# Kernel optimization log

Hardware: AMD Instinct MI355X
Metric: run time of the kernel (lower is better)

The kernel has to match this reference:

```python
import jax, jax.numpy as jnp
import numpy as np

N = 50000   # nodes
E = 800000  # edges before self-loops
H = 4       # heads
D = 64      # num_h_feats (per-head out dim of hidden layers)
C = 2       # num_classes
NEG = 0.2   # DGL GATConv leaky_relu negative_slope
EPS = 1e-5  # BatchNorm eps


def setup_inputs() -> dict:
    key = jax.random.key(0)
    ks = jax.random.split(key, 16)
    inp = {}
    inp['feats'] = jax.random.normal(ks[0], (N, 9), jnp.float32)
    inp['W1'] = jax.random.normal(ks[1], (9, H * D), jnp.float32) * 0.1
    inp['al1'] = jax.random.normal(ks[2], (H, D), jnp.float32) * 0.1
    inp['ar1'] = jax.random.normal(ks[3], (H, D), jnp.float32) * 0.1
    inp['b1'] = jnp.zeros((H, D), jnp.float32)
    inp['Wm'] = jax.random.normal(ks[4], (D, H * D), jnp.float32) * 0.1
    inp['alm'] = jax.random.normal(ks[5], (H, D), jnp.float32) * 0.1
    inp['arm'] = jax.random.normal(ks[6], (H, D), jnp.float32) * 0.1
    inp['bm'] = jnp.zeros((H, D), jnp.float32)
    inp['W2'] = jax.random.normal(ks[7], (D, H * C), jnp.float32) * 0.1
    inp['al2'] = jax.random.normal(ks[8], (H, C), jnp.float32) * 0.1
    inp['ar2'] = jax.random.normal(ks[9], (H, C), jnp.float32) * 0.1
    inp['b2'] = jnp.zeros((H, C), jnp.float32)
    inp['gamma'] = jnp.ones((D,), jnp.float32)
    inp['beta'] = jnp.zeros((D,), jnp.float32)
    inp['src'] = jax.random.randint(ks[10], (E,), 0, N, jnp.int32)
    inp['dst'] = jax.random.randint(ks[11], (E,), 0, N, jnp.int32)
    return inp


def gat_layer(x, W, al, ar, b, src, dst, out_d):
    """DGL GATConv: linear -> per-edge attention -> dst-softmax -> scatter-sum."""
    n = x.shape[0]
    z = (x @ W).reshape(n, H, out_d)                 # [N, H, Dout]
    el = jnp.sum(z * al, axis=-1)                    # [N, H] attn on src
    er = jnp.sum(z * ar, axis=-1)                    # [N, H] attn on dst
    e = jax.nn.leaky_relu(el[src] + er[dst], NEG)    # [E, H]
    m = jax.ops.segment_max(e, dst, num_segments=n)  # per-dst max (stable softmax)
    a = jnp.exp(e - m[dst])
    s = jax.ops.segment_sum(a, dst, num_segments=n)
    alpha = a / s[dst]                               # [E, H]
    out = jax.ops.segment_sum(alpha[:, :, None] * z[src], dst, num_segments=n)
    return out + b                                   # [N, H, Dout]


def batchnorm(h, gamma, beta):
    mu = jnp.mean(h, axis=0)
    var = jnp.var(h, axis=0)
    return (h - mu) * jax.lax.rsqrt(var + EPS) * gamma + beta


def reference(feats, W1, al1, ar1, b1, Wm, alm, arm, bm, W2, al2, ar2, b2,
              gamma, beta, src, dst):
    # dgl.add_self_loop
    loop = jnp.arange(N, dtype=src.dtype)
    s = jnp.concatenate([src, loop])
    d = jnp.concatenate([dst, loop])
    h = gat_layer(feats, W1, al1, ar1, b1, s, d, D).sum(axis=1)  # head-sum
    h = batchnorm(h, gamma, beta)
    h = gat_layer(h, Wm, alm, arm, bm, s, d, D).sum(axis=1)
    h = batchnorm(h, gamma, beta)
    o = gat_layer(h, W2, al2, ar2, b2, s, d, C).sum(axis=1)      # [N, C]
    return o
```

## Files before the change

kernel.cpp:

```cpp
#include <hip/hip_runtime.h>
#include <hip/hip_bf16.h>

typedef __hip_bfloat16 bf16;
typedef __bf16 bf16x8 __attribute__((ext_vector_type(8)));
typedef float f32x4 __attribute__((ext_vector_type(4)));
typedef _Float16 h16;
typedef _Float16 h16x4 __attribute__((ext_vector_type(4)));

#define LOG2E 1.44269504088896340736f

__device__ __forceinline__ float b2f(bf16 v) { return __bfloat162float(v); }

__device__ __forceinline__ float ldin(const void* p, size_t i, int isb) {
    return isb ? b2f(((const bf16*)p)[i]) : ((const float*)p)[i];
}
__device__ __forceinline__ unsigned short f2bfbits(float f) {
    bf16 v = __float2bfloat16(f);
    return *(unsigned short*)&v;
}

__global__ __launch_bounds__(256) void prep_kernel(
    const void* __restrict__ feats, const void* __restrict__ W1, const void* __restrict__ Wm,
    const void* __restrict__ al1, const void* __restrict__ ar1,
    const void* __restrict__ alm, const void* __restrict__ arm,
    const unsigned* __restrict__ gbits,
    const int* __restrict__ dstv, int* __restrict__ deg,
    unsigned short* __restrict__ fpad, unsigned short* __restrict__ W1T,
    unsigned short* __restrict__ WmT,
    float* __restrict__ alf1, float* __restrict__ arf1,
    float* __restrict__ alfm, float* __restrict__ arfm,
    unsigned short* __restrict__ zhs, float* __restrict__ zcs, float* __restrict__ elp,
    int* __restrict__ flag, int Nn, int E) {
    int isb = (gbits[0] == 0x3F803F80u) ? 1 : 0;
    long t = (long)blockIdx.x * 256 + threadIdx.x;
    if (t == 0) *flag = isb;
    long b0 = (long)Nn * 8;
    long b1 = b0 + 2048;
    long b2 = b1 + 2048;
    long b3 = b2 + 256;
    long b4 = b3 + 268;
    long b5 = b4 + E;
    if (t < b0) {
        int s = (int)(t & 7); long n = t >> 3;
        int k0 = s * 8;
        union { unsigned short us[8]; uint4 v; } o;
#pragma unroll
        for (int j = 0; j < 8; j++) {
            int k = k0 + j;
            o.us[j] = (k < 9) ? f2bfbits(ldin(feats, (size_t)n * 9 + k, isb))
                              : (unsigned short)0;
        }
        *(uint4*)(fpad + t * 8) = o.v;
    } else if (t < b1) {
        long u = t - b0;
        int col = (int)(u >> 3), k0 = ((int)u & 7) * 8;
        union { unsigned short us[8]; uint4 v; } o;
#pragma unroll
        for (int j = 0; j < 8; j++) {
            int k = k0 + j;
            o.us[j] = (k < 9) ? f2bfbits(ldin(W1, (size_t)k * 256 + col, isb))
                              : (unsigned short)0;
        }
        *(uint4*)(W1T + u * 8) = o.v;
    } else if (t < b2) {
        long u = t - b1;
        int col = (int)(u >> 3), k0 = ((int)u & 7) * 8;
        union { unsigned short us[8]; uint4 v; } o;
#pragma unroll
        for (int j = 0; j < 8; j++) {
            int k = k0 + j;
            o.us[j] = f2bfbits(ldin(Wm, (size_t)k * 256 + col, isb));
        }
        *(uint4*)(WmT + u * 8) = o.v;
    } else if (t < b3) {
        int u = (int)(t - b2);
        alf1[u] = ldin(al1, u, isb) * LOG2E; arf1[u] = ldin(ar1, u, isb) * LOG2E;
        alfm[u] = ldin(alm, u, isb) * LOG2E; arfm[u] = ldin(arm, u, isb) * LOG2E;
    } else if (t < b4) {
        long u = t - b3;
        if (u < 4) {
            elp[(size_t)Nn * 4 + u] = -1e30f;
        } else if (u < 260) {
            zhs[(size_t)Nn * 256 + (u - 4)] = 0;
        } else {
            zcs[(size_t)Nn * 8 + (u - 260)] = 0.f;
        }
    } else if (t < b5) {
        atomicAdd(&deg[dstv[t - b4]], 1);
    }
}

__global__ __launch_bounds__(256) void scan1_kernel(
    const int* __restrict__ deg, int* __restrict__ off, int* __restrict__ bsum, int Nn) {
    __shared__ int s[256];
    int t = threadIdx.x, i = blockIdx.x * 256 + t;
    int v = (i < Nn) ? ((deg[i] + 3) & ~3) : 0;
    s[t] = v; __syncthreads();
#pragma unroll
    for (int o = 1; o < 256; o <<= 1) {
        int a = (t >= o) ? s[t - o] : 0;
        __syncthreads();
        s[t] += a;
        __syncthreads();
    }
    if (i < Nn) off[i] = s[t];
    if (t == 255) bsum[blockIdx.x] = s[255];
}

__global__ __launch_bounds__(256) void scan2_kernel(int* __restrict__ bsum, int NB) {
    __shared__ int s[256];
    int t = threadIdx.x;
    int v = (t < NB) ? bsum[t] : 0;
    s[t] = v; __syncthreads();
#pragma unroll
    for (int o = 1; o < 256; o <<= 1) {
        int a = (t >= o) ? s[t - o] : 0;
        __syncthreads();
        s[t] += a;
        __syncthreads();
    }
    if (t < NB) bsum[t] = s[t] - v;
}

__global__ __launch_bounds__(256) void scan3_kernel(
    const int* __restrict__ deg, int* __restrict__ off, int* __restrict__ cur,
    int* __restrict__ adj, const int* __restrict__ bsum, int Nn) {
    int i = blockIdx.x * 256 + threadIdx.x;
    if (i < Nn) {
        int d = deg[i], pd = (d + 3) & ~3;
        int ex = off[i] - pd + bsum[i >> 8];
        off[i] = ex;
        cur[i] = ex;
        for (int j = d; j < pd; j++) adj[ex + j] = Nn;
        if (i == Nn - 1) {
            int tot = ex + pd;
            off[Nn] = tot;
#pragma unroll
            for (int j = 0; j < 8; j++) adj[tot + j] = Nn;
        }
    }
}

__global__ __launch_bounds__(256) void scatter_kernel(
    const int* __restrict__ src, const int* __restrict__ dst,
    int* __restrict__ cur, int* __restrict__ adj, int E) {
    int t = blockIdx.x * 256 + threadIdx.x;
    if (t < E) {
        int p = atomicAdd(&cur[dst[t]], 1);
        adj[p] = src[t];
    }
}

__global__ __launch_bounds__(256) void lin_mfma_l1_kernel(
    const unsigned short* __restrict__ xb, const unsigned short* __restrict__ WT,
    const float* __restrict__ alf, const float* __restrict__ arf,
    h16* __restrict__ zh, float* __restrict__ el, float* __restrict__ er, int Nn) {
    __shared__ h16 zs[16 * 256];
    int w = threadIdx.x >> 6;
    int l = threadIdx.x & 63;
    int quad = l >> 4, lc = l & 15;
    int node0 = blockIdx.x * 16;

    int mrow = node0 + lc; if (mrow >= Nn) mrow = Nn - 1;
    const bf16x8* xa = (const bf16x8*)(xb + (size_t)mrow * 64);
    bf16x8 a0 = xa[quad];
    bf16x8 a1 = xa[quad + 4];

    float pe[4] = {0.f, 0.f, 0.f, 0.f}, pr[4] = {0.f, 0.f, 0.f, 0.f};
    int row0 = quad * 4;
#pragma unroll
    for (int ct = 0; ct < 4; ++ct) {
        int col = w * 64 + ct * 16 + lc;
        const bf16x8* wb = (const bf16x8*)(WT + (size_t)col * 64);
        bf16x8 b0 = wb[quad];
        bf16x8 b1 = wb[quad + 4];
        f32x4 c = {0.f, 0.f, 0.f, 0.f};
        c = __builtin_amdgcn_mfma_f32_16x16x32_bf16(a0, b0, c, 0, 0, 0);
        c = __builtin_amdgcn_mfma_f32_16x16x32_bf16(a1, b1, c, 0, 0, 0);
        float av = alf[col], rv = arf[col];
#pragma unroll
        for (int r = 0; r < 4; ++r) {
            pe[r] = fmaf(c[r], av, pe[r]);
            pr[r] = fmaf(c[r], rv, pr[r]);
            zs[(row0 + r) * 256 + col] = (h16)c[r];
        }
    }
#pragma unroll
    for (int o = 1; o < 16; o <<= 1) {
#pragma unroll
        for (int r = 0; r < 4; ++r) {
            pe[r] += __shfl_xor(pe[r], o);
            pr[r] += __shfl_xor(pr[r], o);
        }
    }
    if (lc == 0) {
#pragma unroll
        for (int r = 0; r < 4; ++r) {
            int n = node0 + row0 + r;
            if (n < Nn) { el[n * 4 + w] = pe[r]; er[n * 4 + w] = pr[r]; }
        }
    }
    __syncthreads();
#pragma unroll
    for (int it = 0; it < 2; ++it) {
        int flat = it * 2048 + threadIdx.x * 8;
        int row = flat >> 8;
        if (node0 + row < Nn)
            *(uint4*)(zh + (size_t)node0 * 256 + flat) = *(const uint4*)(zs + flat);
    }
}

__global__ __launch_bounds__(256) void lin_mfma_bn_kernel(
    const float* __restrict__ x,
    const float* __restrict__ bnsum, const float* __restrict__ bnsumsq,
    const void* __restrict__ gamma, const void* __restrict__ beta,
    const unsigned short* __restrict__ WT,
    const float* __restrict__ alf, const float* __restrict__ arf,
    h16* __restrict__ zh, float* __restrict__ el, float* __restrict__ er,
    const int* __restrict__ flag, int Nn) {
    __shared__ h16 zs[16 * 256];
    __shared__ __align__(16) float scs[64], shs[64];
    int tid = threadIdx.x;
    if (tid < 64) {
        int isb = *flag;
        float inv_n = 1.f / (float)Nn;
        float mu = bnsum[tid] * inv_n;
        float var = bnsumsq[tid] * inv_n - mu * mu;
        float s = rsqrtf(var + 1e-5f) * ldin(gamma, tid, isb);
        scs[tid] = s;
        shs[tid] = ldin(beta, tid, isb) - mu * s;
    }
    __syncthreads();

    int w = tid >> 6;
    int l = tid & 63;
    int quad = l >> 4, lc = l & 15;
    int node0 = blockIdx.x * 16;

    int mrow = node0 + lc; if (mrow >= Nn) mrow = Nn - 1;
    const float* xr = x + (size_t)mrow * 64 + quad * 8;
    float4 f0 = ((const float4*)xr)[0];
    float4 f1 = ((const float4*)xr)[1];
    float4 f2 = ((const float4*)(xr + 32))[0];
    float4 f3 = ((const float4*)(xr + 32))[1];
    float4 s0 = ((const float4*)(scs + quad * 8))[0];
    float4 s1 = ((const float4*)(scs + quad * 8))[1];
    float4 s2 = ((const float4*)(scs + 32 + quad * 8))[0];
    float4 s3 = ((const float4*)(scs + 32 + quad * 8))[1];
    float4 h0 = ((const float4*)(shs + quad * 8))[0];
    float4 h1 = ((const float4*)(shs + quad * 8))[1];
    float4 h2 = ((const float4*)(shs + 32 + quad * 8))[0];
    float4 h3 = ((const float4*)(shs + 32 + quad * 8))[1];

    union { bf16x8 v; unsigned short s[8]; } ua, ub;
    ua.s[0] = f2bfbits(fmaf(f0.x, s0.x, h0.x));
    ua.s[1] = f2bfbits(fmaf(f0.y, s0.y, h0.y));
    ua.s[2] = f2bfbits(fmaf(f0.z, s0.z, h0.z));
    ua.s[3] = f2bfbits(fmaf(f0.w, s0.w, h0.w));
    ua.s[4] = f2bfbits(fmaf(f1.x, s1.x, h1.x));
    ua.s[5] = f2bfbits(fmaf(f1.y, s1.y, h1.y));
    ua.s[6] = f2bfbits(fmaf(f1.z, s1.z, h1.z));
    ua.s[7] = f2bfbits(fmaf(f1.w, s1.w, h1.w));
    ub.s[0] = f2bfbits(fmaf(f2.x, s2.x, h2.x));
    ub.s[1] = f2bfbits(fmaf(f2.y, s2.y, h2.y));
    ub.s[2] = f2bfbits(fmaf(f2.z, s2.z, h2.z));
    ub.s[3] = f2bfbits(fmaf(f2.w, s2.w, h2.w));
    ub.s[4] = f2bfbits(fmaf(f3.x, s3.x, h3.x));
    ub.s[5] = f2bfbits(fmaf(f3.y, s3.y, h3.y));
    ub.s[6] = f2bfbits(fmaf(f3.z, s3.z, h3.z));
    ub.s[7] = f2bfbits(fmaf(f3.w, s3.w, h3.w));
    bf16x8 a0 = ua.v, a1 = ub.v;

    float pe[4] = {0.f, 0.f, 0.f, 0.f}, pr[4] = {0.f, 0.f, 0.f, 0.f};
    int row0 = quad * 4;
#pragma unroll
    for (int ct = 0; ct < 4; ++ct) {
        int col = w * 64 + ct * 16 + lc;
        const bf16x8* wb = (const bf16x8*)(WT + (size_t)col * 64);
        bf16x8 b0 = wb[quad];
        bf16x8 b1 = wb[quad + 4];
        f32x4 c = {0.f, 0.f, 0.f, 0.f};
        c = __builtin_amdgcn_mfma_f32_16x16x32_bf16(a0, b0, c, 0, 0, 0);
        c = __builtin_amdgcn_mfma_f32_16x16x32_bf16(a1, b1, c, 0, 0, 0);
        float av = alf[col], rv = arf[col];
#pragma unroll
        for (int r = 0; r < 4; ++r) {
            pe[r] = fmaf(c[r], av, pe[r]);
            pr[r] = fmaf(c[r], rv, pr[r]);
            zs[(row0 + r) * 256 + col] = (h16)c[r];
        }
    }
#pragma unroll
    for (int o = 1; o < 16; o <<= 1) {
#pragma unroll
        for (int r = 0; r < 4; ++r) {
            pe[r] += __shfl_xor(pe[r], o);
            pr[r] += __shfl_xor(pr[r], o);
        }
    }
    if (lc == 0) {
#pragma unroll
        for (int r = 0; r < 4; ++r) {
            int n = node0 + row0 + r;
            if (n < Nn) { el[n * 4 + w] = pe[r]; er[n * 4 + w] = pr[r]; }
        }
    }
    __syncthreads();
#pragma unroll
    for (int it = 0; it < 2; ++it) {
        int flat = it * 2048 + threadIdx.x * 8;
        int row = flat >> 8;
        if (node0 + row < Nn)
            *(uint4*)(zh + (size_t)node0 * 256 + flat) = *(const uint4*)(zs + flat);
    }
}

__global__ __launch_bounds__(256) void bnstats_kernel(
    const float* __restrict__ x, float* __restrict__ bnsum, float* __restrict__ bnsumsq,
    int Nn) {
    __shared__ float ssum[4][64], ssq[4][64];
    int tid = threadIdx.x;
    int d = tid & 63, r = tid >> 6;
    float s = 0.f, q = 0.f;
    int stride = gridDim.x * 4;
    for (int n = blockIdx.x * 4 + r; n < Nn; n += stride) {
        float v = x[(size_t)n * 64 + d];
        s += v;
        q = fmaf(v, v, q);
    }
    ssum[r][d] = s; ssq[r][d] = q;
    __syncthreads();
    if (tid < 64) {
        float ts = ssum[0][tid] + ssum[1][tid] + ssum[2][tid] + ssum[3][tid];
        float tq = ssq[0][tid] + ssq[1][tid] + ssq[2][tid] + ssq[3][tid];
        atomicAdd(&bnsum[tid], ts);
        atomicAdd(&bnsumsq[tid], tq);
    }
}

__global__ __launch_bounds__(256) void lin3_kernel(
    const float* __restrict__ x,
    const float* __restrict__ bnsum, const float* __restrict__ bnsumsq,
    const void* __restrict__ gamma, const void* __restrict__ beta,
    const void* __restrict__ W, const void* __restrict__ al, const void* __restrict__ ar,
    float* __restrict__ zc, float* __restrict__ el, float* __restrict__ er,
    const int* __restrict__ flag, int Nn) {
    __shared__ __align__(16) float scs[64], shs[64];
    int isb = *flag;
    int tid = threadIdx.x;
    if (tid < 64) {
        float inv_n = 1.f / (float)Nn;
        float mu = bnsum[tid] * inv_n;
        float var = bnsumsq[tid] * inv_n - mu * mu;
        float s = rsqrtf(var + 1e-5f) * ldin(gamma, tid, isb);
        scs[tid] = s;
        shs[tid] = ldin(beta, tid, isb) - mu * s;
    }
    __syncthreads();
    int t = blockIdx.x * 256 + tid;
    if (t >= Nn * 4) return;
    int n = t >> 2, h = t & 3;
    const float4* xr4 = (const float4*)(x + (size_t)n * 64);
    float a0 = 0.f, a1 = 0.f;
#pragma unroll 4
    for (int kk = 0; kk < 16; kk++) {
        float4 xv = xr4[kk];
        int k = kk * 4;
        float xn;
        xn = fmaf(xv.x, scs[k + 0], shs[k + 0]);
        a0 += xn * ldin(W, (k + 0) * 8 + h * 2, isb);
        a1 += xn * ldin(W, (k + 0) * 8 + h * 2 + 1, isb);
        xn = fmaf(xv.y, scs[k + 1], shs[k + 1]);
        a0 += xn * ldin(W, (k + 1) * 8 + h * 2, isb);
        a1 += xn * ldin(W, (k + 1) * 8 + h * 2 + 1, isb);
        xn = fmaf(xv.z, scs[k + 2], shs[k + 2]);
        a0 += xn * ldin(W, (k + 2) * 8 + h * 2, isb);
        a1 += xn * ldin(W, (k + 2) * 8 + h * 2 + 1, isb);
        xn = fmaf(xv.w, scs[k + 3], shs[k + 3]);
        a0 += xn * ldin(W, (k + 3) * 8 + h * 2, isb);
        a1 += xn * ldin(W, (k + 3) * 8 + h * 2 + 1, isb);
    }
    zc[n * 8 + h * 2 + 0] = a0;
    zc[n * 8 + h * 2 + 1] = a1;
    el[t] = (a0 * ldin(al, h * 2, isb) + a1 * ldin(al, h * 2 + 1, isb)) * LOG2E;
    er[t] = (a0 * ldin(ar, h * 2, isb) + a1 * ldin(ar, h * 2 + 1, isb)) * LOG2E;
}

#define GATH(ev, zv, sv)                                        \
    {                                                           \
        ev[0] = el[sv.x * 4 + h]; ev[1] = el[sv.y * 4 + h];     \
        ev[2] = el[sv.z * 4 + h]; ev[3] = el[sv.w * 4 + h];     \
        zv[0] = zrow[(size_t)sv.x * 64 + l];                    \
        zv[1] = zrow[(size_t)sv.y * 64 + l];                    \
        zv[2] = zrow[(size_t)sv.z * 64 + l];                    \
        zv[3] = zrow[(size_t)sv.w * 64 + l];                    \
    }
#define COMP(ev, zv)                                        \
    {                                                       \
        _Pragma("unroll") for (int j = 0; j < 4; j++) {     \
            float e = ev[j] + ern;                          \
            e = fmaxf(e, 0.2f * e);                         \
            float wj = __builtin_amdgcn_exp2f(e);           \
            lsum += wj;                                     \
            acc.x = fmaf(wj, (float)zv[j].x, acc.x);        \
            acc.y = fmaf(wj, (float)zv[j].y, acc.y);        \
            acc.z = fmaf(wj, (float)zv[j].z, acc.z);        \
            acc.w = fmaf(wj, (float)zv[j].w, acc.w);        \
        }                                                   \
    }

__global__ __launch_bounds__(256) void gat_agg64_kernel(
    const h16* __restrict__ zh, const float* __restrict__ el, const float* __restrict__ er,
    const int* __restrict__ off, const int* __restrict__ adj, const void* __restrict__ bias,
    float* __restrict__ x, const int* __restrict__ flag, int Nn, int total_waves) {
    int isb = *flag;
    int tid = threadIdx.x;
    int l = tid & 63;
    int h = l >> 4;
    int gw = blockIdx.x * 4 + (tid >> 6);
    const h16x4* zrow = (const h16x4*)zh;

    float4 bsl;
    bsl.x = ldin(bias, l * 4 + 0, isb);
    bsl.y = ldin(bias, l * 4 + 1, isb);
    bsl.z = ldin(bias, l * 4 + 2, isb);
    bsl.w = ldin(bias, l * 4 + 3, isb);

    if (gw >= Nn) return;

    int n = gw;
    int fs0 = off[n], fs1 = off[n + 1];
    float fel = el[n * 4 + h], fer = er[n * 4 + h];
    int4 fsv = *(const int4*)(adj + fs0);

    while (true) {
        int s0 = fs0;
        int nb = (fs1 - fs0) >> 2;
        float eln = fel, ern = fer;
        int4 svA = fsv;
        h16x4 zself = zrow[(size_t)n * 64 + l];
        int nn = n + total_waves;
        if (nn < Nn) {
            fs0 = off[nn]; fs1 = off[nn + 1];
            fel = el[nn * 4 + h]; fer = er[nn * 4 + h];
            fsv = *(const int4*)(adj + fs0);
        }

        float e0 = eln + ern;
        e0 = fmaxf(e0, 0.2f * e0);
        float w0 = __builtin_amdgcn_exp2f(e0);
        float lsum = w0;
        float4 acc = {0.f, 0.f, 0.f, 0.f};

        if (nb > 0) {
            float evA[4], evB[4];
            h16x4 zvA[4], zvB[4];
            GATH(evA, zvA, svA);
            int4 svB = *(const int4*)(adj + s0 + 4);
            int k = 0;
            while (true) {
                if (k + 1 < nb) GATH(evB, zvB, svB);
                svA = *(const int4*)(adj + s0 + (k + 2) * 4);
                COMP(evA, zvA);
                if (++k >= nb) break;
                if (k + 1 < nb) GATH(evA, zvA, svA);
                svB = *(const int4*)(adj + s0 + (k + 2) * 4);
                COMP(evB, zvB);
                if (++k >= nb) break;
            }
        }

        acc.x = fmaf(w0, (float)zself.x, acc.x);
        acc.y = fmaf(w0, (float)zself.y, acc.y);
        acc.z = fmaf(w0, (float)zself.z, acc.z);
        acc.w = fmaf(w0, (float)zself.w, acc.w);

        float inv = 1.f / lsum;
        float4 r;
        r.x = fmaf(acc.x, inv, bsl.x);
        r.y = fmaf(acc.y, inv, bsl.y);
        r.z = fmaf(acc.z, inv, bsl.z);
        r.w = fmaf(acc.w, inv, bsl.w);
#pragma unroll
        for (int o = 16; o < 64; o <<= 1) {
            r.x += __shfl_xor(r.x, o);
            r.y += __shfl_xor(r.y, o);
            r.z += __shfl_xor(r.z, o);
            r.w += __shfl_xor(r.w, o);
        }
        if (h == 0) ((float4*)(x + (size_t)n * 64))[l & 15] = r;
        if (nn >= Nn) break;
        n = nn;
    }
}
#undef GATH
#undef COMP

__global__ __launch_bounds__(256) void gat_agg2_kernel(
    const float* __restrict__ zc, const float* __restrict__ el, const float* __restrict__ er,
    const int* __restrict__ off, const int* __restrict__ adj, const void* __restrict__ bias,
    void* __restrict__ out, const int* __restrict__ flag, int Nn) {
    int isb = *flag;
    int t = blockIdx.x * 256 + threadIdx.x;
    if (t >= Nn * 4) return;
    int n = t >> 2, h = t & 3;
    const float2* zc2 = (const float2*)zc;
    float er_nh = er[n * 4 + h];
    float e0 = el[n * 4 + h] + er_nh;
    e0 = fmaxf(e0, 0.2f * e0);
    float w0 = __builtin_amdgcn_exp2f(e0);
    float lsum = w0;
    float2 zn = zc2[n * 4 + h];
    float a0 = w0 * zn.x, a1 = w0 * zn.y;
    int s0 = off[n], s1 = off[n + 1];
    for (int i = s0; i < s1; i += 4) {
        int4 sv = *(const int4*)(adj + i);
        float ev[4]; float2 zj[4];
        ev[0] = el[sv.x * 4 + h]; zj[0] = zc2[sv.x * 4 + h];
        ev[1] = el[sv.y * 4 + h]; zj[1] = zc2[sv.y * 4 + h];
        ev[2] = el[sv.z * 4 + h]; zj[2] = zc2[sv.z * 4 + h];
        ev[3] = el[sv.w * 4 + h]; zj[3] = zc2[sv.w * 4 + h];
#pragma unroll
        for (int j = 0; j < 4; j++) {
            float e = ev[j] + er_nh;
            e = fmaxf(e, 0.2f * e);
            float w = __builtin_amdgcn_exp2f(e);
            lsum += w;
            a0 = fmaf(w, zj[j].x, a0);
            a1 = fmaf(w, zj[j].y, a1);
        }
    }
    float inv = 1.f / lsum;
    float v0 = fmaf(a0, inv, ldin(bias, h * 2 + 0, isb));
    float v1 = fmaf(a1, inv, ldin(bias, h * 2 + 1, isb));
#pragma unroll
    for (int o = 1; o < 4; o <<= 1) {
        v0 += __shfl_xor(v0, o);
        v1 += __shfl_xor(v1, o);
    }
    if (h == 0) {
        if (isb) {
            ((bf16*)out)[n * 2 + 0] = __float2bfloat16(v0);
            ((bf16*)out)[n * 2 + 1] = __float2bfloat16(v1);
        } else {
            ((float*)out)[n * 2 + 0] = v0;
            ((float*)out)[n * 2 + 1] = v1;
        }
    }
}

extern "C" void kernel_launch(void* const* d_in, const int* in_sizes, int n_in,
                              void* d_out, int out_size, void* d_ws, size_t ws_size,
                              hipStream_t stream) {
    const void* feats = d_in[0];
    const void* W1    = d_in[1];
    const void* al1   = d_in[2];
    const void* ar1   = d_in[3];
    const void* b1    = d_in[4];
    const void* Wm    = d_in[5];
    const void* alm   = d_in[6];
    const void* arm   = d_in[7];
    const void* bm    = d_in[8];
    const void* W2    = d_in[9];
    const void* al2   = d_in[10];
    const void* ar2   = d_in[11];
    const void* b2v   = d_in[12];
    const void* gamma = d_in[13];
    const void* beta  = d_in[14];
    const int*  src   = (const int*)d_in[15];
    const int*  dst   = (const int*)d_in[16];

    int Nn = in_sizes[0] / 9;
    int E  = in_sizes[15];

    float* ws = (float*)d_ws;
    h16*   zh   = (h16*)ws;
    float* zc   = ws + (size_t)(Nn + 1) * 128;
    float* el   = zc + (size_t)Nn * 8 + 8;
    float* er   = el + (size_t)Nn * 4 + 4;
    float* x    = er + (size_t)Nn * 4;
    int*   deg  = (int*)(x + (size_t)Nn * 64);
    float* bns1 = (float*)(deg + Nn);
    float* bnq1 = bns1 + 64;
    float* bns2 = bnq1 + 64;
    float* bnq2 = bns2 + 64;
    size_t msetBytes = (size_t)Nn * 4 + 256 * 4;
    float* alf1 = bnq2 + 64;
    float* arf1 = alf1 + 256;
    float* alfm = arf1 + 256;
    float* arfm = alfm + 256;
    unsigned short* fpad =
        (unsigned short*)(((uintptr_t)(arfm + 256) + 15) & ~(uintptr_t)15);
    unsigned short* W1T  = fpad + (size_t)Nn * 64;
    unsigned short* WmT  = W1T + 256 * 64;
    int*   flag = (int*)(WmT + 256 * 64);
    int*   off  = flag + 1;
    int*   cur  = off + Nn + 1;
    int*   adj  = (int*)(((uintptr_t)(cur + Nn) + 15) & ~(uintptr_t)15);
    int*   bsum = adj + E + 3 * Nn + 8;

    dim3 B(256);
    int NB1 = (Nn + 255) / 256;
    int gE  = (E + 255) / 256;
    int gMF = (Nn + 15) / 16;
    int gN4 = (Nn * 4 + 255) / 256;
    long prepN = (long)Nn * 8 + 2048 + 2048 + 256 + 268 + E;
    int gPrep = (int)((prepN + 255) / 256);
    int AGG_GRID = 2048;
    int total_waves = AGG_GRID * 4;

    hipMemsetAsync(deg, 0, msetBytes, stream);

    prep_kernel<<<gPrep, B, 0, stream>>>(feats, W1, Wm, al1, ar1, alm, arm,
                                         (const unsigned*)gamma, dst, deg,
                                         fpad, W1T, WmT,
                                         alf1, arf1, alfm, arfm,
                                         (unsigned short*)zh, zc, el, flag, Nn, E);

    scan1_kernel<<<NB1, B, 0, stream>>>(deg, off, bsum, Nn);
    scan2_kernel<<<1, B, 0, stream>>>(bsum, NB1);
    scan3_kernel<<<NB1, B, 0, stream>>>(deg, off, cur, adj, bsum, Nn);
    scatter_kernel<<<gE, B, 0, stream>>>(src, dst, cur, adj, E);

    lin_mfma_l1_kernel<<<gMF, B, 0, stream>>>(fpad, W1T, alf1, arf1, zh, el, er, Nn);
    gat_agg64_kernel<<<AGG_GRID, B, 0, stream>>>(
        zh, el, er, off, adj, b1, x, flag, Nn, total_waves);
    bnstats_kernel<<<512, B, 0, stream>>>(x, bns1, bnq1, Nn);

    lin_mfma_bn_kernel<<<gMF, B, 0, stream>>>(x, bns1, bnq1, gamma, beta,
                                              WmT, alfm, arfm, zh, el, er, flag, Nn);
    gat_agg64_kernel<<<AGG_GRID, B, 0, stream>>>(
        zh, el, er, off, adj, bm, x, flag, Nn, total_waves);
    bnstats_kernel<<<512, B, 0, stream>>>(x, bns2, bnq2, Nn);

    lin3_kernel<<<gN4, B, 0, stream>>>(x, bns2, bnq2, gamma, beta,
                                       W2, al2, ar2, zc, el, er, flag, Nn);
    gat_agg2_kernel<<<gN4, B, 0, stream>>>(zc, el, er, off, adj, b2v, d_out, flag, Nn);
}
```

Measured before the change: 450.7 us.

## Deepen gather prefetch, fuse scan stages, and double aggregation grid

Fuses the block-sum scan into the offset-fixup kernel, so each block redundantly rescans the block sums and one launch is dropped. Extends the software-pipelined neighbour gather in the 64-wide aggregation from double to triple buffering and applies the same three-deep pipeline to the 2-class aggregation. Doubles the persistent aggregation grid and enlarges the adjacency tail padding to cover the deeper prefetch reads. In exchange, the deeper buffers raise register pressure, which may reduce occupancy.

Result: no change. 448.8 us (-0.4%).

```diff
diff --git a/kernel.cpp b/kernel.cpp
--- a/kernel.cpp
+++ b/kernel.cpp
@@ -107,7 +107,9 @@
     if (t == 255) bsum[blockIdx.x] = s[255];
 }
 
-__global__ __launch_bounds__(256) void scan2_kernel(int* __restrict__ bsum, int NB) {
+__global__ __launch_bounds__(256) void scan3_kernel(
+    const int* __restrict__ deg, int* __restrict__ off, int* __restrict__ cur,
+    int* __restrict__ adj, const int* __restrict__ bsum, int Nn, int NB) {
     __shared__ int s[256];
     int t = threadIdx.x;
     int v = (t < NB) ? bsum[t] : 0;
@@ -119,24 +121,20 @@
         s[t] += a;
         __syncthreads();
     }
-    if (t < NB) bsum[t] = s[t] - v;
-}
-
-__global__ __launch_bounds__(256) void scan3_kernel(
-    const int* __restrict__ deg, int* __restrict__ off, int* __restrict__ cur,
-    int* __restrict__ adj, const int* __restrict__ bsum, int Nn) {
-    int i = blockIdx.x * 256 + threadIdx.x;
+    s[t] -= v;
+    __syncthreads();
+    int base = s[blockIdx.x];
+    int i = blockIdx.x * 256 + t;
     if (i < Nn) {
         int d = deg[i], pd = (d + 3) & ~3;
-        int ex = off[i] - pd + bsum[i >> 8];
+        int ex = off[i] - pd + base;
         off[i] = ex;
         cur[i] = ex;
         for (int j = d; j < pd; j++) adj[ex + j] = Nn;
         if (i == Nn - 1) {
             int tot = ex + pd;
             off[Nn] = tot;
-#pragma unroll
-            for (int j = 0; j < 8; j++) adj[tot + j] = Nn;
+            for (int j = 0; j < 32; j++) adj[tot + j] = Nn;
         }
     }
 }
@@ -453,19 +451,25 @@
         float4 acc = {0.f, 0.f, 0.f, 0.f};
 
         if (nb > 0) {
-            float evA[4], evB[4];
-            h16x4 zvA[4], zvB[4];
+            float evA[4], evB[4], evC[4];
+            h16x4 zvA[4], zvB[4], zvC[4];
             GATH(evA, zvA, svA);
             int4 svB = *(const int4*)(adj + s0 + 4);
+            if (nb > 1) GATH(evB, zvB, svB);
+            int4 svC = *(const int4*)(adj + s0 + 8);
             int k = 0;
             while (true) {
-                if (k + 1 < nb) GATH(evB, zvB, svB);
-                svA = *(const int4*)(adj + s0 + (k + 2) * 4);
+                if (k + 2 < nb) GATH(evC, zvC, svC);
+                svA = *(const int4*)(adj + s0 + (k + 3) * 4);
                 COMP(evA, zvA);
                 if (++k >= nb) break;
-                if (k + 1 < nb) GATH(evA, zvA, svA);
-                svB = *(const int4*)(adj + s0 + (k + 2) * 4);
+                if (k + 2 < nb) GATH(evA, zvA, svA);
+                svB = *(const int4*)(adj + s0 + (k + 3) * 4);
                 COMP(evB, zvB);
+                if (++k >= nb) break;
+                if (k + 2 < nb) GATH(evB, zvB, svB);
+                svC = *(const int4*)(adj + s0 + (k + 3) * 4);
+                COMP(evC, zvC);
                 if (++k >= nb) break;
             }
         }
@@ -495,6 +499,25 @@
 }
 #undef GATH
 #undef COMP
+
+#define GATH2(ev, zv, sv)                                       \
+    {                                                           \
+        ev[0] = el[sv.x * 4 + h]; zv[0] = zc2[sv.x * 4 + h];    \
+        ev[1] = el[sv.y * 4 + h]; zv[1] = zc2[sv.y * 4 + h];    \
+        ev[2] = el[sv.z * 4 + h]; zv[2] = zc2[sv.z * 4 + h];    \
+        ev[3] = el[sv.w * 4 + h]; zv[3] = zc2[sv.w * 4 + h];    \
+    }
+#define COMP2(ev, zv)                                       \
+    {                                                       \
+        _Pragma("unroll") for (int j = 0; j < 4; j++) {     \
+            float e = ev[j] + er_nh;                        \
+            e = fmaxf(e, 0.2f * e);                         \
+            float w = __builtin_amdgcn_exp2f(e);            \
+            lsum += w;                                      \
+            a0 = fmaf(w, zv[j].x, a0);                      \
+            a1 = fmaf(w, zv[j].y, a1);                      \
+        }                                                   \
+    }
 
 __global__ __launch_bounds__(256) void gat_agg2_kernel(
     const float* __restrict__ zc, const float* __restrict__ el, const float* __restrict__ er,
@@ -512,22 +535,30 @@
     float lsum = w0;
     float2 zn = zc2[n * 4 + h];
     float a0 = w0 * zn.x, a1 = w0 * zn.y;
-    int s0 = off[n], s1 = off[n + 1];
-    for (int i = s0; i < s1; i += 4) {
-        int4 sv = *(const int4*)(adj + i);
-        float ev[4]; float2 zj[4];
-        ev[0] = el[sv.x * 4 + h]; zj[0] = zc2[sv.x * 4 + h];
-        ev[1] = el[sv.y * 4 + h]; zj[1] = zc2[sv.y * 4 + h];
-        ev[2] = el[sv.z * 4 + h]; zj[2] = zc2[sv.z * 4 + h];
-        ev[3] = el[sv.w * 4 + h]; zj[3] = zc2[sv.w * 4 + h];
-#pragma unroll
-        for (int j = 0; j < 4; j++) {
-            float e = ev[j] + er_nh;
-            e = fmaxf(e, 0.2f * e);
-            float w = __builtin_amdgcn_exp2f(e);
-            lsum += w;
-            a0 = fmaf(w, zj[j].x, a0);
-            a1 = fmaf(w, zj[j].y, a1);
+    int s0 = off[n];
+    int nb = (off[n + 1] - s0) >> 2;
+    if (nb > 0) {
+        float evA[4], evB[4], evC[4];
+        float2 zvA[4], zvB[4], zvC[4];
+        int4 svA = *(const int4*)(adj + s0);
+        GATH2(evA, zvA, svA);
+        int4 svB = *(const int4*)(adj + s0 + 4);
+        if (nb > 1) GATH2(evB, zvB, svB);
+        int4 svC = *(const int4*)(adj + s0 + 8);
+        int k = 0;
+        while (true) {
+            if (k + 2 < nb) GATH2(evC, zvC, svC);
+            svA = *(const int4*)(adj + s0 + (k + 3) * 4);
+            COMP2(evA, zvA);
+            if (++k >= nb) break;
+            if (k + 2 < nb) GATH2(evA, zvA, svA);
+            svB = *(const int4*)(adj + s0 + (k + 3) * 4);
+            COMP2(evB, zvB);
+            if (++k >= nb) break;
+            if (k + 2 < nb) GATH2(evB, zvB, svB);
+            svC = *(const int4*)(adj + s0 + (k + 3) * 4);
+            COMP2(evC, zvC);
+            if (++k >= nb) break;
         }
     }
     float inv = 1.f / lsum;
@@ -548,6 +579,8 @@
         }
     }
 }
+#undef GATH2
+#undef COMP2
 
 extern "C" void kernel_launch(void* const* d_in, const int* in_sizes, int n_in,
                               void* d_out, int out_size, void* d_ws, size_t ws_size,
@@ -597,7 +630,7 @@
     int*   off  = flag + 1;
     int*   cur  = off + Nn + 1;
     int*   adj  = (int*)(((uintptr_t)(cur + Nn) + 15) & ~(uintptr_t)15);
-    int*   bsum = adj + E + 3 * Nn + 8;
+    int*   bsum = adj + E + 3 * Nn + 32;
 
     dim3 B(256);
     int NB1 = (Nn + 255) / 256;
@@ -606,7 +639,7 @@
     int gN4 = (Nn * 4 + 255) / 256;
     long prepN = (long)Nn * 8 + 2048 + 2048 + 256 + 268 + E;
     int gPrep = (int)((prepN + 255) / 256);
-    int AGG_GRID = 2048;
+    int AGG_GRID = 4096;
     int total_waves = AGG_GRID * 4;
 
     hipMemsetAsync(deg, 0, msetBytes, stream);
@@ -618,8 +651,7 @@
                                          (unsigned short*)zh, zc, el, flag, Nn, E);
 
     scan1_kernel<<<NB1, B, 0, stream>>>(deg, off, bsum, Nn);
-    scan2_kernel<<<1, B, 0, stream>>>(bsum, NB1);
-    scan3_kernel<<<NB1, B, 0, stream>>>(deg, off, cur, adj, bsum, Nn);
+    scan3_kernel<<<NB1, B, 0, stream>>>(deg, off, cur, adj, bsum, Nn, NB1);
     scatter_kernel<<<gE, B, 0, stream>>>(src, dst, cur, adj, E);
 
     lin_mfma_l1_kernel<<<gMF, B, 0, stream>>>(fpad, W1T, alf1, arf1, zh, el, er, Nn);
```
